# Optimization experiments

Hardware: AMD Instinct MI355X
Metric: run time of the kernel (lower is better)

The kernel has to match this reference:

```python
import jax, jax.numpy as jnp
import numpy as np

DIM, HEADS, WS, SHIFT, H, W = 512, 16, 8, 4, 64, 64
N = WS * WS
HD = DIM // HEADS
SCALE = HD ** -0.5
MLP_HID = 4 * DIM
TIME_DIM = 512
NW = (H // WS) * (W // WS)


def _rel_pos_index(ws):
    ch, cw = np.meshgrid(np.arange(ws), np.arange(ws), indexing='ij')
    cf = np.stack([ch, cw]).reshape(2, -1)          # [2, N]
    rc = (cf[:, :, None] - cf[:, None, :]).transpose(1, 2, 0)  # [N,N,2]
    rc[..., 0] += ws - 1
    rc[..., 1] += ws - 1
    rc[..., 0] *= 2 * ws - 1
    return rc.sum(-1)                                # [N, N] int


def _attn_mask(h, w, ws, ss):
    img = np.zeros((h, w))
    sl = (slice(0, -ws), slice(-ws, -ss), slice(-ss, None))
    cnt = 0
    for hs in sl:
        for wsl in sl:
            img[hs, wsl] = cnt
            cnt += 1
    mw = img.reshape(h // ws, ws, w // ws, ws).transpose(0, 2, 1, 3).reshape(-1, ws * ws)
    am = mw[:, None, :] - mw[:, :, None]             # [nW, N, N]
    return np.where(am != 0, -100.0, 0.0).astype(np.float32)

RPI = _rel_pos_index(WS)
MASK = jnp.asarray(_attn_mask(H, W, WS, SHIFT))


def window_partition(x, ws):
    B, h, w, C = x.shape
    x = x.reshape(B, h // ws, ws, w // ws, ws, C).transpose(0, 1, 3, 2, 4, 5)
    return x.reshape(-1, ws * ws, C)


def window_reverse(win, ws, h, w):
    B = win.shape[0] // ((h // ws) * (w // ws))
    x = win.reshape(B, h // ws, w // ws, ws, ws, -1).transpose(0, 1, 3, 2, 4, 5)
    return x.reshape(B, h, w, -1)


def layernorm(x, g, b, eps=1e-5):
    m = jnp.mean(x, axis=-1, keepdims=True)
    v = jnp.mean(jnp.square(x - m), axis=-1, keepdims=True)
    return (x - m) * jax.lax.rsqrt(v + eps) * g + b


def setup_inputs():
    key = jax.random.key(0)
    ks = jax.random.split(key, 12)
    s = 0.02
    return {
        'x': jax.random.normal(ks[0], (16, H, W, DIM), jnp.float32),
        't_emb': jax.random.normal(ks[1], (16, TIME_DIM), jnp.float32),
        'norm1_g': jnp.ones((DIM,), jnp.float32),
        'norm1_b': jnp.zeros((DIM,), jnp.float32),
        'qkv_w': jax.random.normal(ks[2], (3 * DIM, DIM), jnp.float32) * s,
        'qkv_b': jnp.zeros((3 * DIM,), jnp.float32),
        'proj_w': jax.random.normal(ks[3], (DIM, DIM), jnp.float32) * s,
        'proj_b': jnp.zeros((DIM,), jnp.float32),
        'rpb_table': jax.random.normal(ks[4], ((2 * WS - 1) ** 2, HEADS), jnp.float32) * s,
        'norm2_g': jnp.ones((DIM,), jnp.float32),
        'norm2_b': jnp.zeros((DIM,), jnp.float32),
        'fc1_w': jax.random.normal(ks[5], (MLP_HID, DIM), jnp.float32) * s,
        'fc1_b': jnp.zeros((MLP_HID,), jnp.float32),
        'fc2_w': jax.random.normal(ks[6], (DIM, MLP_HID), jnp.float32) * s,
        'fc2_b': jnp.zeros((DIM,), jnp.float32),
        'ada_w': jax.random.normal(ks[7], (4 * DIM, TIME_DIM), jnp.float32) * s,
        'ada_b': jnp.zeros((4 * DIM,), jnp.float32),
    }


def reference(x, t_emb, norm1_g, norm1_b, qkv_w, qkv_b, proj_w, proj_b,
              rpb_table, norm2_g, norm2_b, fc1_w, fc1_b, fc2_w, fc2_b,
              ada_w, ada_b):
    B = x.shape[0]
    ada = jax.nn.silu(t_emb) @ ada_w.T + ada_b           # [B, 4*dim]
    shift1, scale1, shift2, scale2 = jnp.split(ada, 4, axis=-1)

    shortcut = x
    h = layernorm(x, norm1_g, norm1_b)
    h = h * (1.0 + scale1[:, None, None, :]) + shift1[:, None, None, :]
    h = jnp.roll(h, (-SHIFT, -SHIFT), axis=(1, 2))
    xw = window_partition(h, WS)                          # [B*nW, N, C]
    B_ = xw.shape[0]

    qkv = xw @ qkv_w.T + qkv_b                            # [B_, N, 3C]
    qkv = qkv.reshape(B_, N, 3, HEADS, HD).transpose(2, 0, 3, 1, 4)
    q, k, v = qkv[0], qkv[1], qkv[2]                      # [B_, Hh, N, hd]
    attn = jnp.einsum('bhnd,bhmd->bhnm', q * SCALE, k)    # [B_, Hh, N, N]

    bias = rpb_table[RPI.reshape(-1)].reshape(N, N, HEADS).transpose(2, 0, 1)
    attn = attn + bias[None]
    attn = attn.reshape(B, NW, HEADS, N, N) + MASK[None, :, None]
    attn = jax.nn.softmax(attn.reshape(B_, HEADS, N, N), axis=-1)

    out = jnp.einsum('bhnm,bhmd->bhnd', attn, v)
    out = out.transpose(0, 2, 1, 3).reshape(B_, N, DIM)
    out = out @ proj_w.T + proj_b

    h = window_reverse(out, WS, H, W)
    h = jnp.roll(h, (SHIFT, SHIFT), axis=(1, 2))
    x = shortcut + h

    shortcut = x
    h = layernorm(x, norm2_g, norm2_b)
    h = h * (1.0 + scale2[:, None, None, :]) + shift2[:, None, None, :]
    h = jax.nn.gelu(h @ fc1_w.T + fc1_b, approximate=False)
    h = h @ fc2_w.T + fc2_b
    return shortcut + h
```

## Files before the change

kernel.cpp:

```cpp
#include <hip/hip_runtime.h>
#include <cstdint>
#include <cstddef>

typedef __bf16 bf16x8 __attribute__((ext_vector_type(8)));
typedef float f32x4 __attribute__((ext_vector_type(4)));
typedef unsigned short u16x8 __attribute__((ext_vector_type(8)));
typedef unsigned short u16x4 __attribute__((ext_vector_type(4)));

#define DEV __device__ __forceinline__

DEV unsigned short f2b(float f) {
    __bf16 b = (__bf16)f;
    return __builtin_bit_cast(unsigned short, b);
}

DEV float gelu_f(float v) {
    float u = 0.7978845608f * v * fmaf(0.044715f, v * v, 1.f);
    float e = __expf(2.f * u);
    float th = 1.f - 2.f / (e + 1.f);
    return 0.5f * v * (1.f + th);
}

__global__ __launch_bounds__(256) void cvt_all(const float* __restrict__ s0, const float* __restrict__ s1,
                                               const float* __restrict__ s2, const float* __restrict__ s3,
                                               unsigned short* __restrict__ d0, unsigned short* __restrict__ d1,
                                               unsigned short* __restrict__ d2, unsigned short* __restrict__ d3) {
    int b = blockIdx.x;
    const float* s; unsigned short* d; int lb;
    if (b < 768)       { s = s0; d = d0; lb = b; }
    else if (b < 1024) { s = s1; d = d1; lb = b - 768; }
    else if (b < 2048) { s = s2; d = d2; lb = b - 1024; }
    else               { s = s3; d = d3; lb = b - 2048; }
    int i = lb * 256 + threadIdx.x;
    float4 f = ((const float4*)s)[i];
    u16x4 o;
    o[0] = f2b(f.x); o[1] = f2b(f.y); o[2] = f2b(f.z); o[3] = f2b(f.w);
    ((u16x4*)d)[i] = o;
}

__global__ __launch_bounds__(256) void bias_pre(const float* __restrict__ rpb, float* __restrict__ bias) {
    int idx = blockIdx.x * 256 + threadIdx.x;
    int h = idx >> 12, ij = idx & 4095;
    int i = ij >> 6, j = ij & 63;
    int r = ((i >> 3) - (j >> 3) + 7) * 15 + ((i & 7) - (j & 7) + 7);
    bias[idx] = rpb[r * 16 + h];
}

__global__ __launch_bounds__(256) void ada_kernel(const float* __restrict__ t_emb,
                                                  const float* __restrict__ aw,
                                                  const float* __restrict__ ab,
                                                  float* __restrict__ ada) {
    __shared__ float st[512];
    int b = blockIdx.x, jc = blockIdx.y;
    for (int k = threadIdx.x; k < 512; k += 256) {
        float t = t_emb[b * 512 + k];
        st[k] = t / (1.f + __expf(-t));
    }
    __syncthreads();
    int j = jc * 256 + threadIdx.x;
    const float* wr = aw + (size_t)j * 512;
    float acc = ab[j];
    for (int k = 0; k < 512; ++k) acc += st[k] * wr[k];
    ada[b * 2048 + j] = acc;
}

template <int WIN>
__global__ __launch_bounds__(256, 4) void ln_mod(const float* __restrict__ xin,
                                                 const float* __restrict__ g,
                                                 const float* __restrict__ beta,
                                                 const float* __restrict__ ada,
                                                 unsigned short* __restrict__ out) {
    int wv = threadIdx.x >> 6, l = threadIdx.x & 63;
    int tok = blockIdx.x * 4 + wv;
    int bb;
    const float* src;
    if (WIN) {
        int w = tok >> 6, t = tok & 63;
        bb = w >> 6;
        int nw = w & 63;
        int y = (((nw >> 3) << 3) + (t >> 3) + 4) & 63;
        int x = (((nw & 7) << 3) + (t & 7) + 4) & 63;
        src = xin + ((size_t)(bb * 64 + y) * 64 + x) * 512;
    } else {
        bb = tok >> 12;
        src = xin + (size_t)tok * 512;
    }
    const float4* f4 = (const float4*)src;
    float4 v0 = f4[l * 2];
    float4 v1 = f4[l * 2 + 1];
    float s = v0.x + v0.y + v0.z + v0.w + v1.x + v1.y + v1.z + v1.w;
    float ss = v0.x * v0.x + v0.y * v0.y + v0.z * v0.z + v0.w * v0.w +
               v1.x * v1.x + v1.y * v1.y + v1.z * v1.z + v1.w * v1.w;
#pragma unroll
    for (int d = 1; d < 64; d <<= 1) {
        s += __shfl_xor(s, d, 64);
        ss += __shfl_xor(ss, d, 64);
    }
    float mean = s * (1.f / 512.f);
    float var = ss * (1.f / 512.f) - mean * mean;
    float rstd = rsqrtf(var + 1e-5f);
    const float* sh = ada + bb * 2048 + (WIN ? 0 : 1024);
    const float* sc = ada + bb * 2048 + (WIN ? 512 : 1536);
    int c = l * 8;
    u16x8 o;
#pragma unroll
    for (int q = 0; q < 8; ++q) {
        float xv = (q < 4) ? (&v0.x)[q] : (&v1.x)[q - 4];
        float nv = (xv - mean) * rstd * g[c + q] + beta[c + q];
        nv = nv * (1.f + sc[c + q]) + sh[c + q];
        o[q] = f2b(nv);
    }
    *(u16x8*)(out + (size_t)tok * 512 + c) = o;
}

template <int EPI>
__global__ __launch_bounds__(256, 4) void gemm_bt(const unsigned short* __restrict__ A,
                                                  const unsigned short* __restrict__ B,
                                                  const float* __restrict__ bias,
                                                  void* __restrict__ outv,
                                                  const float* __restrict__ resid,
                                                  int N, int K, int m0g, int nbx) {
    __shared__ __align__(16) unsigned short sA[128 * 64];
    __shared__ __align__(16) unsigned short sB[128 * 64];
    const int tid = threadIdx.x;
    const int cpx = gridDim.x >> 3;
    const int wg = (blockIdx.x & 7) * cpx + (blockIdx.x >> 3);
    const int by = wg / nbx, bx = wg - by * nbx;
    const int bm = by * 128, bn = bx * 128;
    const int l = tid & 63, wv = tid >> 6;
    const int wm = (wv >> 1) * 64, wn = (wv & 1) * 64;
    const int lrow = l & 15, lg = l >> 4;

    auto stage = [&](int k0) {
#pragma unroll
        for (int inst = 0; inst < 4; ++inst) {
            int S = inst * 256 + tid;
            int r = S >> 3, j = S & 7;
            int c0 = j ^ (r & 7);
            const unsigned short* gA = A + (size_t)(bm + r) * K + k0 + c0 * 8;
            __builtin_amdgcn_global_load_lds((const __attribute__((address_space(1))) void*)gA,
                                             (__attribute__((address_space(3))) void*)&sA[S * 8], 16, 0, 0);
        }
#pragma unroll
        for (int inst = 0; inst < 4; ++inst) {
            int S = inst * 256 + tid;
            int r = S >> 3, j = S & 7;
            int c0 = j ^ (r & 7);
            const unsigned short* gB = B + (size_t)(bn + r) * K + k0 + c0 * 8;
            __builtin_amdgcn_global_load_lds((const __attribute__((address_space(1))) void*)gB,
                                             (__attribute__((address_space(3))) void*)&sB[S * 8], 16, 0, 0);
        }
    };

    f32x4 acc[4][4] = {};
    const int nk = K >> 6;
    stage(0);
    for (int kt = 0; kt < nk; ++kt) {
        __syncthreads();
        {
            bf16x8 a0[4], b0[4];
#pragma unroll
            for (int m = 0; m < 4; ++m) {
                int R = wm + m * 16 + lrow;
                a0[m] = *(const bf16x8*)(sA + R * 64 + ((lg ^ (R & 7)) * 8));
            }
#pragma unroll
            for (int n = 0; n < 4; ++n) {
                int C = wn + n * 16 + lrow;
                b0[n] = *(const bf16x8*)(sB + C * 64 + ((lg ^ (C & 7)) * 8));
            }
#pragma unroll
            for (int m = 0; m < 4; ++m)
#pragma unroll
                for (int n = 0; n < 4; ++n)
                    acc[m][n] = __builtin_amdgcn_mfma_f32_16x16x32_bf16(a0[m], b0[n], acc[m][n], 0, 0, 0);
        }
        bf16x8 a1[4], b1[4];
#pragma unroll
        for (int m = 0; m < 4; ++m) {
            int R = wm + m * 16 + lrow;
            a1[m] = *(const bf16x8*)(sA + R * 64 + (((4 | lg) ^ (R & 7)) * 8));
        }
#pragma unroll
        for (int n = 0; n < 4; ++n) {
            int C = wn + n * 16 + lrow;
            b1[n] = *(const bf16x8*)(sB + C * 64 + (((4 | lg) ^ (C & 7)) * 8));
        }
        __syncthreads();
        if (kt + 1 < nk) stage((kt + 1) * 64);
#pragma unroll
        for (int m = 0; m < 4; ++m)
#pragma unroll
            for (int n = 0; n < 4; ++n)
                acc[m][n] = __builtin_amdgcn_mfma_f32_16x16x32_bf16(a1[m], b1[n], acc[m][n], 0, 0, 0);
    }

    if constexpr (EPI == 0 || EPI == 1 || EPI == 4) {
        unsigned short* o = (unsigned short*)outv;
        unsigned short* tb = &sA[0] + wv * 1152;
        float bv[4];
#pragma unroll
        for (int n = 0; n < 4; ++n) bv[n] = bias[bn + wn + n * 16 + lrow];
#pragma unroll
        for (int m = 0; m < 4; ++m) {
#pragma unroll
            for (int n = 0; n < 4; ++n)
#pragma unroll
                for (int r = 0; r < 4; ++r) {
                    float v = acc[m][n][r] + bv[n];
                    if constexpr (EPI == 1) v = gelu_f(v);
                    tb[(lg * 4 + r) * 72 + n * 16 + lrow] = f2b(v);
                }
#pragma unroll
            for (int it = 0; it < 2; ++it) {
                int rr = it * 8 + (l >> 3);
                int cc = (l & 7) * 8;
                u16x8 vv = *(const u16x8*)(tb + rr * 72 + cc);
                if constexpr (EPI == 4) {
                    int row = bm + wm + m * 16 + rr;
                    int col = bn + wn + cc;
                    int w_ = row >> 6, t_ = row & 63;
                    size_t dst = (size_t)w_ * 98304 + (size_t)(col >> 9) * 32768 +
                                 (size_t)((col >> 5) & 15) * 2048 + t_ * 32 + (col & 31);
                    *(u16x8*)(o + dst) = vv;
                } else {
                    *(u16x8*)(o + (size_t)(bm + wm + m * 16 + rr) * N + bn + wn + cc) = vv;
                }
            }
        }
    } else if constexpr (EPI == 2) {
        float* o = (float*)outv;
#pragma unroll
        for (int m = 0; m < 4; ++m)
#pragma unroll
            for (int r = 0; r < 4; ++r) {
                int row = bm + wm + m * 16 + lg * 4 + r;
                int wdx = row >> 6, t = row & 63;
                int bb = wdx >> 6, nw = wdx & 63;
                int Y = (((nw >> 3) << 3) + (t >> 3) + 4) & 63;
                int X = (((nw & 7) << 3) + (t & 7) + 4) & 63;
                size_t base = ((size_t)(bb * 64 + Y) * 64 + X) * 512;
#pragma unroll
                for (int n = 0; n < 4; ++n) {
                    int col = bn + wn + n * 16 + lrow;
                    o[base + col] = resid[base + col] + acc[m][n][r] + bias[col];
                }
            }
    } else {
        float* o = (float*)outv;
#pragma unroll
        for (int m = 0; m < 4; ++m)
#pragma unroll
            for (int r = 0; r < 4; ++r) {
                size_t rg = (size_t)(m0g + bm + wm + m * 16 + lg * 4 + r) * 512;
#pragma unroll
                for (int n = 0; n < 4; ++n) {
                    int col = bn + wn + n * 16 + lrow;
                    o[rg + col] += acc[m][n][r] + bias[col];
                }
            }
    }
}

__global__ __launch_bounds__(256, 2) void attn_kernel(const unsigned short* __restrict__ qkv,
                                                      const float* __restrict__ bias_t,
                                                      unsigned short* __restrict__ out) {
    __shared__ __align__(16) unsigned short P_lds[4][64 * 72];
    __shared__ __align__(16) unsigned short Vt[4][32 * 72];
    const int wv = threadIdx.x >> 6, l = threadIdx.x & 63;
    const int u = blockIdx.x * 4 + wv;
    const int w = u >> 4, h = u & 15;
    const int lrow = l & 15, lg = l >> 4;
    const float SCALE = 0.17677669529663687f;

    const unsigned short* qb = qkv + (size_t)w * 98304 + (size_t)h * 2048;

    bf16x8 qf[4], kf[4];
#pragma unroll
    for (int i = 0; i < 4; ++i) {
        qf[i] = *(const bf16x8*)(qb + (16 * i + lrow) * 32 + lg * 8);
        kf[i] = *(const bf16x8*)(qb + 32768 + (16 * i + lrow) * 32 + lg * 8);
    }
    f32x4 S[4][4] = {};
#pragma unroll
    for (int mi = 0; mi < 4; ++mi)
#pragma unroll
        for (int ni = 0; ni < 4; ++ni)
            S[mi][ni] = __builtin_amdgcn_mfma_f32_16x16x32_bf16(qf[mi], kf[ni], S[mi][ni], 0, 0, 0);

    u16x8 vreg[4];
    const unsigned short* vp = qb + 65536 + (size_t)l * 32;
#pragma unroll
    for (int d0 = 0; d0 < 4; ++d0) vreg[d0] = *(const u16x8*)(vp + d0 * 8);

    const int nw = w & 63;
    const int wh0 = (nw >> 3) << 3, ww0 = (nw & 7) << 3;
    auto region = [&](int t) -> int {
        int yy = wh0 + (t >> 3), xx = ww0 + (t & 7);
        int rh = (yy < 56) ? 0 : ((yy < 60) ? 1 : 2);
        int rw = (xx < 56) ? 0 : ((xx < 60) ? 1 : 2);
        return rh * 3 + rw;
    };
    int jreg[4], jcol[4];
#pragma unroll
    for (int ni = 0; ni < 4; ++ni) {
        jcol[ni] = 16 * ni + lrow;
        jreg[ni] = region(jcol[ni]);
    }
    const float* bh = bias_t + h * 4096;
    unsigned short* pl = &P_lds[wv][0];
#pragma unroll
    for (int mi = 0; mi < 4; ++mi)
#pragma unroll
        for (int r = 0; r < 4; ++r) {
            int i = 16 * mi + 4 * lg + r;
            int ireg = region(i);
            const float* bi = bh + i * 64;
            float pv[4];
            float mx = -1e30f;
#pragma unroll
            for (int ni = 0; ni < 4; ++ni) {
                float val = S[mi][ni][r] * SCALE + bi[jcol[ni]];
                if (ireg != jreg[ni]) val -= 100.f;
                pv[ni] = val;
                mx = fmaxf(mx, val);
            }
#pragma unroll
            for (int d = 1; d < 16; d <<= 1) mx = fmaxf(mx, __shfl_xor(mx, d, 64));
            float sum = 0.f;
#pragma unroll
            for (int ni = 0; ni < 4; ++ni) {
                pv[ni] = __expf(pv[ni] - mx);
                sum += pv[ni];
            }
#pragma unroll
            for (int d = 1; d < 16; d <<= 1) sum += __shfl_xor(sum, d, 64);
            float inv = 1.f / sum;
#pragma unroll
            for (int ni = 0; ni < 4; ++ni) pl[i * 72 + jcol[ni]] = f2b(pv[ni] * inv);
        }

    unsigned short* vt = &Vt[wv][0];
#pragma unroll
    for (int d0 = 0; d0 < 4; ++d0)
#pragma unroll
        for (int q = 0; q < 8; ++q) vt[(d0 * 8 + q) * 72 + l] = vreg[d0][q];

    __syncthreads();

    f32x4 O[4][2] = {};
#pragma unroll
    for (int ks = 0; ks < 2; ++ks) {
        bf16x8 pa[4], vb[2];
#pragma unroll
        for (int mi = 0; mi < 4; ++mi)
            pa[mi] = *(const bf16x8*)(pl + (16 * mi + lrow) * 72 + ks * 32 + lg * 8);
#pragma unroll
        for (int ni = 0; ni < 2; ++ni)
            vb[ni] = *(const bf16x8*)(vt + (16 * ni + lrow) * 72 + ks * 32 + lg * 8);
#pragma unroll
        for (int mi = 0; mi < 4; ++mi)
#pragma unroll
            for (int ni = 0; ni < 2; ++ni)
                O[mi][ni] = __builtin_amdgcn_mfma_f32_16x16x32_bf16(pa[mi], vb[ni], O[mi][ni], 0, 0, 0);
    }

    unsigned short* ostg = pl;
#pragma unroll
    for (int mi = 0; mi < 4; ++mi)
#pragma unroll
        for (int ni = 0; ni < 2; ++ni)
#pragma unroll
            for (int r = 0; r < 4; ++r)
                ostg[(16 * mi + 4 * lg + r) * 40 + 16 * ni + lrow] = f2b(O[mi][ni][r]);
    unsigned short* op = out + (size_t)(w * 64 + l) * 512 + h * 32;
#pragma unroll
    for (int q4 = 0; q4 < 4; ++q4)
        *(u16x8*)(op + q4 * 8) = *(const u16x8*)(ostg + l * 40 + q4 * 8);
}

extern "C" void kernel_launch(void* const* d_in, const int* in_sizes, int n_in,
                              void* d_out, int out_size, void* d_ws, size_t ws_size,
                              hipStream_t stream) {
    const float* x      = (const float*)d_in[0];
    const float* t_emb  = (const float*)d_in[1];
    const float* n1g    = (const float*)d_in[2];
    const float* n1b    = (const float*)d_in[3];
    const float* qkv_w  = (const float*)d_in[4];
    const float* qkv_b  = (const float*)d_in[5];
    const float* proj_w = (const float*)d_in[6];
    const float* proj_b = (const float*)d_in[7];
    const float* rpb    = (const float*)d_in[8];
    const float* n2g    = (const float*)d_in[9];
    const float* n2b    = (const float*)d_in[10];
    const float* fc1_w  = (const float*)d_in[11];
    const float* fc1_b  = (const float*)d_in[12];
    const float* fc2_w  = (const float*)d_in[13];
    const float* fc2_b  = (const float*)d_in[14];
    const float* ada_w  = (const float*)d_in[15];
    const float* ada_b  = (const float*)d_in[16];
    float* out = (float*)d_out;

    char* p = (char*)d_ws;
    auto alloc = [&](size_t bytes) { void* r = (void*)p; p += (bytes + 255) & ~(size_t)255; return r; };
    unsigned short* Wq  = (unsigned short*)alloc((size_t)1536 * 512 * 2);
    unsigned short* Wp  = (unsigned short*)alloc((size_t)512 * 512 * 2);
    unsigned short* W1  = (unsigned short*)alloc((size_t)2048 * 512 * 2);
    unsigned short* W2  = (unsigned short*)alloc((size_t)512 * 2048 * 2);
    float*          bias_t = (float*)alloc((size_t)16 * 4096 * 4);
    float*          ada = (float*)alloc((size_t)16 * 2048 * 4);
    unsigned short* bufA = (unsigned short*)alloc((size_t)65536 * 512 * 2);
    unsigned short* bufB = (unsigned short*)alloc((size_t)65536 * 1536 * 2);

    cvt_all<<<3072, 256, 0, stream>>>(qkv_w, proj_w, fc1_w, fc2_w, Wq, Wp, W1, W2);
    bias_pre<<<256, 256, 0, stream>>>(rpb, bias_t);
    ada_kernel<<<dim3(16, 8), 256, 0, stream>>>(t_emb, ada_w, ada_b, ada);
    ln_mod<1><<<16384, 256, 0, stream>>>(x, n1g, n1b, ada, bufA);
    gemm_bt<4><<<6144, 256, 0, stream>>>(bufA, Wq, qkv_b, bufB, nullptr, 1536, 512, 0, 12);
    attn_kernel<<<4096, 256, 0, stream>>>(bufB, bias_t, bufA);
    gemm_bt<2><<<2048, 256, 0, stream>>>(bufA, Wp, proj_b, out, x, 512, 512, 0, 4);
    ln_mod<0><<<16384, 256, 0, stream>>>(out, n2g, n2b, ada, bufA);
    for (int c = 0; c < 2; ++c) {
        gemm_bt<1><<<4096, 256, 0, stream>>>(bufA + (size_t)c * 32768 * 512, W1, fc1_b,
                                             bufB, nullptr, 2048, 512, 0, 16);
        gemm_bt<3><<<1024, 256, 0, stream>>>(bufB, W2, fc2_b, out, nullptr,
                                             512, 2048, c * 32768, 4);
    }
}
```

Baseline: 775.7 us.

## Load GEMM B operand directly from global into registers, bypassing LDS

The B (weight) tile is no longer staged through shared memory. Each wave now reads its B fragments straight from global memory into registers every k-step. This halves LDS usage per block, which could allow higher occupancy, and removes the LDS writes and reads for B. In exchange, B is no longer shared between the two waves that use the same columns, so global/L2 traffic for B doubles, and the global loads sit on the critical path with no prefetch ahead of the MFMAs.

```diff
diff --git a/kernel.cpp b/kernel.cpp
--- a/kernel.cpp
+++ b/kernel.cpp
@@ -121,7 +121,6 @@
                                                   const float* __restrict__ resid,
                                                   int N, int K, int m0g, int nbx) {
     __shared__ __align__(16) unsigned short sA[128 * 64];
-    __shared__ __align__(16) unsigned short sB[128 * 64];
     const int tid = threadIdx.x;
     const int cpx = gridDim.x >> 3;
     const int wg = (blockIdx.x & 7) * cpx + (blockIdx.x >> 3);
@@ -131,7 +130,7 @@
     const int wm = (wv >> 1) * 64, wn = (wv & 1) * 64;
     const int lrow = l & 15, lg = l >> 4;
 
-    auto stage = [&](int k0) {
+    auto stageA = [&](int k0) {
 #pragma unroll
         for (int inst = 0; inst < 4; ++inst) {
             int S = inst * 256 + tid;
@@ -141,53 +140,42 @@
             __builtin_amdgcn_global_load_lds((const __attribute__((address_space(1))) void*)gA,
                                              (__attribute__((address_space(3))) void*)&sA[S * 8], 16, 0, 0);
         }
-#pragma unroll
-        for (int inst = 0; inst < 4; ++inst) {
-            int S = inst * 256 + tid;
-            int r = S >> 3, j = S & 7;
-            int c0 = j ^ (r & 7);
-            const unsigned short* gB = B + (size_t)(bn + r) * K + k0 + c0 * 8;
-            __builtin_amdgcn_global_load_lds((const __attribute__((address_space(1))) void*)gB,
-                                             (__attribute__((address_space(3))) void*)&sB[S * 8], 16, 0, 0);
-        }
     };
 
     f32x4 acc[4][4] = {};
     const int nk = K >> 6;
-    stage(0);
+    stageA(0);
+    const unsigned short* Bl = B + (size_t)(bn + wn + lrow) * K + lg * 8;
     for (int kt = 0; kt < nk; ++kt) {
+        bf16x8 b0[4], b1[4];
+#pragma unroll
+        for (int n = 0; n < 4; ++n) {
+            const unsigned short* bp = Bl + (size_t)n * 16 * K + kt * 64;
+            b0[n] = *(const bf16x8*)(bp);
+            b1[n] = *(const bf16x8*)(bp + 32);
+        }
         __syncthreads();
         {
-            bf16x8 a0[4], b0[4];
+            bf16x8 a0[4];
 #pragma unroll
             for (int m = 0; m < 4; ++m) {
                 int R = wm + m * 16 + lrow;
                 a0[m] = *(const bf16x8*)(sA + R * 64 + ((lg ^ (R & 7)) * 8));
             }
 #pragma unroll
-            for (int n = 0; n < 4; ++n) {
-                int C = wn + n * 16 + lrow;
-                b0[n] = *(const bf16x8*)(sB + C * 64 + ((lg ^ (C & 7)) * 8));
-            }
-#pragma unroll
             for (int m = 0; m < 4; ++m)
 #pragma unroll
                 for (int n = 0; n < 4; ++n)
                     acc[m][n] = __builtin_amdgcn_mfma_f32_16x16x32_bf16(a0[m], b0[n], acc[m][n], 0, 0, 0);
         }
-        bf16x8 a1[4], b1[4];
+        bf16x8 a1[4];
 #pragma unroll
         for (int m = 0; m < 4; ++m) {
             int R = wm + m * 16 + lrow;
             a1[m] = *(const bf16x8*)(sA + R * 64 + (((4 | lg) ^ (R & 7)) * 8));
         }
-#pragma unroll
-        for (int n = 0; n < 4; ++n) {
-            int C = wn + n * 16 + lrow;
-            b1[n] = *(const bf16x8*)(sB + C * 64 + (((4 | lg) ^ (C & 7)) * 8));
-        }
         __syncthreads();
-        if (kt + 1 < nk) stage((kt + 1) * 64);
+        if (kt + 1 < nk) stageA((kt + 1) * 64);
 #pragma unroll
         for (int m = 0; m < 4; ++m)
 #pragma unroll
```

Measured after the change: 1.110 ms. +43.0%, slower.
